# Kernel optimization log

Measured on AMD Instinct MI355X. Metric: run time of the kernel, lower is better.

Reference implementation:

```python
import jax, jax.numpy as jnp
import numpy as np

B, S, D, H = 2, 2048, 1024, 16
HD = D // H  # head_dim = 64


def setup_inputs() -> dict:
    key = jax.random.key(0)
    ks = jax.random.split(key, 6)
    scale = 1.0 / np.sqrt(D)
    x = jax.random.normal(ks[0], (B, S, D), dtype=jnp.float32)
    W_in = jax.random.normal(ks[1], (D, D), dtype=jnp.float32) * scale
    b_in = jnp.zeros((D,), dtype=jnp.float32)
    # per-head causal sequence-mixing weight, (H, S, S)
    W_mix = jax.random.normal(ks[2], (H, S, S), dtype=jnp.float32) / np.sqrt(S)
    W_out = jax.random.normal(ks[3], (D, D), dtype=jnp.float32) * scale
    b_out = jnp.zeros((D,), dtype=jnp.float32)
    index = S - 1  # python int; parallel form computes all indices at once
    return {"x": x, "W_in": W_in, "b_in": b_in, "W_mix": W_mix,
            "W_out": W_out, "b_out": b_out, "index": index}


def reference(x, W_in, b_in, W_mix, W_out, b_out, index):
    # in-projection (token-wise dense)
    xp = x @ W_in.T + b_in                      # (B, S, D)
    xh = xp.reshape(B, S, H, HD)                # split heads
    # causal (lower-triangular) per-head mixing over sequence positions
    causal = jnp.tril(jnp.ones((S, S), dtype=x.dtype))
    Wm = W_mix * causal                         # (H, S, S)
    # out[b,t,h,:] = sum_{j<=t} Wm[h,t,j] * xh[b,j,h,:]
    mixed = jnp.einsum('htj,bjhd->bthd', Wm, xh)
    out = mixed.reshape(B, S, D) @ W_out.T + b_out
    return out
```

## Files before the change

### kernel.cpp

```cpp
#include <hip/hip_runtime.h>
#include <hip/hip_bf16.h>
#include <stdint.h>

#define B_ 2
#define S_ 2048
#define D_ 1024
#define H_ 16
#define HD_ 64

typedef __attribute__((ext_vector_type(8))) short short8v;
typedef __attribute__((ext_vector_type(4))) float f32x4;
typedef __attribute__((ext_vector_type(4))) int int4v;

__device__ __forceinline__ unsigned short f2bf(float f) {
  union { float f; unsigned int u; } c; c.f = f;
  unsigned int u = c.u;
  unsigned int r = u + 0x7FFFu + ((u >> 16) & 1u);
  return (unsigned short)(r >> 16);
}

__device__ __forceinline__ void gload16(const void* g, void* l) {
  __builtin_amdgcn_global_load_lds(
      (const __attribute__((address_space(1))) unsigned int*)g,
      (__attribute__((address_space(3))) unsigned int*)l, 16, 0, 0);
}

#define NX4_ (B_ * S_ * D_ / 4)
#define NW4_ (D_ * D_ / 4)
__global__ __launch_bounds__(256) void convert3(
    const float* __restrict__ x, const float* __restrict__ wi, const float* __restrict__ wo,
    unsigned short* __restrict__ xb, unsigned short* __restrict__ wib,
    unsigned short* __restrict__ wob) {
  int i = blockIdx.x * 256 + threadIdx.x;
  const float* src; unsigned short* dst; int j;
  if (i < NX4_)              { src = x;  dst = xb;  j = i; }
  else if (i < NX4_ + NW4_)  { src = wi; dst = wib; j = i - NX4_; }
  else                       { src = wo; dst = wob; j = i - NX4_ - NW4_; }
  float4 v = reinterpret_cast<const float4*>(src)[j];
  ushort4 o;
  o.x = f2bf(v.x); o.y = f2bf(v.y); o.z = f2bf(v.z); o.w = f2bf(v.w);
  reinterpret_cast<ushort4*>(dst)[j] = o;
}

template<bool OUT_BF16>
__global__ __launch_bounds__(256) void gemm_bt(
    const unsigned short* __restrict__ A,
    const unsigned short* __restrict__ Bm,
    const float* __restrict__ bias,
    void* __restrict__ Cout,
    int M, int N, int K)
{
  __shared__ unsigned short As[128 * 32];
  __shared__ unsigned short Bs[128 * 32];
  const int tid = threadIdx.x;
  const int bM = blockIdx.y * 128, bN = blockIdx.x * 128;
  const int lane = tid & 63;
  const int w = tid >> 6;
  const int wr = (w >> 1) * 64;
  const int wc = (w & 1) * 64;
  const int lr = lane & 15, lk = (lane >> 4) * 8;
  const int srA = w * 32 + (lane >> 2);
  const int scs = (lane & 3) * 8;

  f32x4 acc[4][4] = {};

  for (int k0 = 0; k0 < K; k0 += 32) {
    gload16(A + (size_t)(bM + srA) * K + k0 + scs,      &As[srA * 32 + scs]);
    gload16(A + (size_t)(bM + srA + 16) * K + k0 + scs, &As[(srA + 16) * 32 + scs]);
    gload16(Bm + (size_t)(bN + srA) * K + k0 + scs,      &Bs[srA * 32 + scs]);
    gload16(Bm + (size_t)(bN + srA + 16) * K + k0 + scs, &Bs[(srA + 16) * 32 + scs]);
    __syncthreads();
    short8v av[4], bv[4];
#pragma unroll
    for (int m = 0; m < 4; m++)
      av[m] = *reinterpret_cast<const short8v*>(&As[(wr + m * 16 + lr) * 32 + lk]);
#pragma unroll
    for (int n = 0; n < 4; n++)
      bv[n] = *reinterpret_cast<const short8v*>(&Bs[(wc + n * 16 + lr) * 32 + lk]);
#pragma unroll
    for (int m = 0; m < 4; m++)
#pragma unroll
      for (int n = 0; n < 4; n++)
        acc[m][n] = __builtin_amdgcn_mfma_f32_16x16x32_bf16(av[m], bv[n], acc[m][n], 0, 0, 0);
    __syncthreads();
  }

  const int r0 = wr + (lane >> 4) * 4;
  const int c0 = wc + lr;
#pragma unroll
  for (int m = 0; m < 4; m++) {
#pragma unroll
    for (int n = 0; n < 4; n++) {
      const int gc = bN + c0 + n * 16;
      const float bb = bias[gc];
#pragma unroll
      for (int j = 0; j < 4; j++) {
        const int gr = bM + r0 + m * 16 + j;
        float v = acc[m][n][j] + bb;
        if (OUT_BF16)
          reinterpret_cast<unsigned short*>(Cout)[(size_t)gr * N + gc] = f2bf(v);
        else
          reinterpret_cast<float*>(Cout)[(size_t)gr * N + gc] = v;
      }
    }
  }
}

__global__ __launch_bounds__(256) void transpose_heads(
    const unsigned short* __restrict__ xp,
    unsigned short* __restrict__ xhT)
{
  const int bh = blockIdx.y;
  const int t0 = blockIdx.x * 64;
  const int b = bh >> 4, h = bh & 15;
  __shared__ unsigned short tile[64][72];
  const int tid = threadIdx.x;
  const int c8 = (tid & 7) * 8;
  const int r = tid >> 3;
  const size_t inBase = ((size_t)(b * S_ + t0)) * D_ + h * HD_;
#pragma unroll
  for (int p = 0; p < 2; p++) {
    const int tt = r + p * 32;
    *reinterpret_cast<int4v*>(&tile[tt][c8]) =
        *reinterpret_cast<const int4v*>(&xp[inBase + (size_t)tt * D_ + c8]);
  }
  __syncthreads();
#pragma unroll
  for (int p = 0; p < 2; p++) {
    const int d = r + p * 32;
    short8v v;
#pragma unroll
    for (int i = 0; i < 8; i++) v[i] = (short)tile[c8 + i][d];
    *reinterpret_cast<short8v*>(&xhT[((size_t)(bh * HD_) + d) * S_ + t0 + c8]) = v;
  }
}

template<bool MASK>
__device__ __forceinline__ short8v mix_fragA(const float* Asf, int rl, int lk, int k0, int T0) {
  f32x4 f0 = *reinterpret_cast<const f32x4*>(&Asf[rl * 32 + lk]);
  f32x4 f1 = *reinterpret_cast<const f32x4*>(&Asf[rl * 32 + lk + 4]);
  const int t = T0 + rl;
  short8v a;
#pragma unroll
  for (int e = 0; e < 4; e++) {
    float v0 = f0[e], v1 = f1[e];
    if (MASK) {
      if (k0 + lk + e > t)     v0 = 0.0f;
      if (k0 + lk + 4 + e > t) v1 = 0.0f;
    }
    a[e]     = (short)f2bf(v0);
    a[4 + e] = (short)f2bf(v1);
  }
  return a;
}

template<bool MASK>
__device__ __forceinline__ void mix_step(
    const float* Asf, const unsigned short* Bs, f32x4 (&acc)[2][4],
    int wr, int wc, int lr, int lk, int k0, int T0) {
  short8v av[2], bv[4];
#pragma unroll
  for (int m = 0; m < 2; m++)
    av[m] = mix_fragA<MASK>(Asf, wr + m * 16 + lr, lk, k0, T0);
#pragma unroll
  for (int n = 0; n < 4; n++)
    bv[n] = *reinterpret_cast<const short8v*>(&Bs[(wc + n * 16 + lr) * 32 + lk]);
#pragma unroll
  for (int m = 0; m < 2; m++)
#pragma unroll
    for (int n = 0; n < 4; n++)
      acc[m][n] = __builtin_amdgcn_mfma_f32_16x16x32_bf16(av[m], bv[n], acc[m][n], 0, 0, 0);
}

__global__ __launch_bounds__(256) void gemm_mix(
    const float* __restrict__ Wmix,
    const unsigned short* __restrict__ xhT,
    unsigned short* __restrict__ mixed)
{
  __shared__ float Asf[64 * 32];
  __shared__ unsigned short Bs[128 * 32];
  const int tid = threadIdx.x;
  const int h = blockIdx.y;
  const int xi = blockIdx.x;
  const int tilei = (xi & 1) ? (31 - (xi >> 1)) : (xi >> 1);
  const int T0 = tilei * 64;
  const int lane = tid & 63;
  const int w = tid >> 6;
  const int wr = (w >> 1) * 32;
  const int wc = (w & 1) * 64;
  const int lr = lane & 15, lk = (lane >> 4) * 8;
  const int arA = w * 16 + (lane >> 3);
  const int acf = (lane & 7) * 4;
  const int brA = w * 32 + (lane >> 2);
  const int bcs = (lane & 3) * 8;
  const int br0 = ((brA >> 6) * H_ + h) * HD_ + (brA & 63);
  const int br1 = (((brA + 16) >> 6) * H_ + h) * HD_ + ((brA + 16) & 63);

  f32x4 acc[2][4] = {};
  const float* Wh = Wmix + (size_t)h * S_ * S_;

  const int kMax = T0 + 64;
  for (int k0 = 0; k0 < kMax; k0 += 32) {
    gload16(Wh + (size_t)(T0 + arA) * S_ + k0 + acf,     &Asf[arA * 32 + acf]);
    gload16(Wh + (size_t)(T0 + arA + 8) * S_ + k0 + acf, &Asf[(arA + 8) * 32 + acf]);
    gload16(xhT + (size_t)br0 * S_ + k0 + bcs, &Bs[brA * 32 + bcs]);
    gload16(xhT + (size_t)br1 * S_ + k0 + bcs, &Bs[(brA + 16) * 32 + bcs]);
    __syncthreads();
    if (k0 + 32 > T0)
      mix_step<true>(Asf, Bs, acc, wr, wc, lr, lk, k0, T0);
    else
      mix_step<false>(Asf, Bs, acc, wr, wc, lr, lk, k0, T0);
    __syncthreads();
  }

  const int r0 = wr + (lane >> 4) * 4;
  const int c0 = wc + lr;
#pragma unroll
  for (int m = 0; m < 2; m++)
#pragma unroll
    for (int n = 0; n < 4; n++) {
      const int cc = c0 + n * 16;
      const int bb = cc >> 6, dd = cc & 63;
#pragma unroll
      for (int j = 0; j < 4; j++) {
        const int tt = T0 + r0 + m * 16 + j;
        mixed[((size_t)(bb * S_ + tt)) * D_ + h * HD_ + dd] = f2bf(acc[m][n][j]);
      }
    }
}

extern "C" void kernel_launch(void* const* d_in, const int* in_sizes, int n_in,
                              void* d_out, int out_size, void* d_ws, size_t ws_size,
                              hipStream_t stream) {
  const float* x     = (const float*)d_in[0];
  const float* W_in  = (const float*)d_in[1];
  const float* b_in  = (const float*)d_in[2];
  const float* W_mix = (const float*)d_in[3];
  const float* W_out = (const float*)d_in[4];
  const float* b_out = (const float*)d_in[5];

  char* ws = (char*)d_ws;
  unsigned short* xb    = (unsigned short*)(ws);
  unsigned short* xp    = (unsigned short*)(ws + 8u * 1024u * 1024u);
  unsigned short* wib   = (unsigned short*)(ws + 16u * 1024u * 1024u);
  unsigned short* wob   = (unsigned short*)(ws + 18u * 1024u * 1024u);
  unsigned short* xhT   = xb;
  unsigned short* mixed = xp;

  convert3<<<dim3((NX4_ + 2 * NW4_) / 256), dim3(256), 0, stream>>>(
      x, W_in, W_out, xb, wib, wob);

  gemm_bt<true><<<dim3(D_ / 128, B_ * S_ / 128), dim3(256), 0, stream>>>(
      xb, wib, b_in, (void*)xp, B_ * S_, D_, D_);

  transpose_heads<<<dim3(S_ / 64, B_ * H_), dim3(256), 0, stream>>>(xp, xhT);

  gemm_mix<<<dim3(S_ / 64, H_), dim3(256), 0, stream>>>(W_mix, xhT, mixed);

  gemm_bt<false><<<dim3(D_ / 128, B_ * S_ / 128), dim3(256), 0, stream>>>(
      mixed, wob, b_out, (void*)d_out, B_ * S_, D_, D_);
}
```

Baseline: 471.6 us.

## Drop LDS staging in GEMMs and fuse head transpose into in-projection

Replaces the LDS-staged GEMMs with register-only kernels that load MFMA fragments directly from global memory, using smaller 64x64 tiles. The in-projection now computes the transposed product W_in·x^T, so its output is already in the head-transposed layout and the separate transpose kernel is removed. The mixing kernel uses 32-row tiles with direct global loads and only masks the final diagonal step. The goal is to cut LDS traffic, barriers and one launch, at the cost of losing cross-wave operand reuse, which means many more redundant global and L2 reads, plus smaller per-wave tiles.

```diff
diff --git a/kernel.cpp b/kernel.cpp
--- a/kernel.cpp
+++ b/kernel.cpp
@@ -10,7 +10,6 @@
 
 typedef __attribute__((ext_vector_type(8))) short short8v;
 typedef __attribute__((ext_vector_type(4))) float f32x4;
-typedef __attribute__((ext_vector_type(4))) int int4v;
 
 __device__ __forceinline__ unsigned short f2bf(float f) {
   union { float f; unsigned int u; } c; c.f = f;
@@ -19,10 +18,8 @@
   return (unsigned short)(r >> 16);
 }
 
-__device__ __forceinline__ void gload16(const void* g, void* l) {
-  __builtin_amdgcn_global_load_lds(
-      (const __attribute__((address_space(1))) unsigned int*)g,
-      (__attribute__((address_space(3))) unsigned int*)l, 16, 0, 0);
+__device__ __forceinline__ f32x4 mfma16(short8v a, short8v b, f32x4 c) {
+  return __builtin_amdgcn_mfma_f32_16x16x32_bf16(a, b, c, 0, 0, 0);
 }
 
 #define NX4_ (B_ * S_ * D_ / 4)
@@ -42,61 +39,50 @@
   reinterpret_cast<ushort4*>(dst)[j] = o;
 }
 
-template<bool OUT_BF16>
-__global__ __launch_bounds__(256) void gemm_bt(
+template<bool OUT_BF16, bool BIAS_ROW>
+__global__ __launch_bounds__(256) void gemm_nolds(
     const unsigned short* __restrict__ A,
     const unsigned short* __restrict__ Bm,
     const float* __restrict__ bias,
-    void* __restrict__ Cout,
-    int M, int N, int K)
+    void* __restrict__ Cout, int M, int N, int K)
 {
-  __shared__ unsigned short As[128 * 32];
-  __shared__ unsigned short Bs[128 * 32];
   const int tid = threadIdx.x;
-  const int bM = blockIdx.y * 128, bN = blockIdx.x * 128;
   const int lane = tid & 63;
   const int w = tid >> 6;
-  const int wr = (w >> 1) * 64;
-  const int wc = (w & 1) * 64;
+  const int bM = blockIdx.y * 64, bN = blockIdx.x * 64;
+  const int wr = (w >> 1) * 32, wc = (w & 1) * 32;
   const int lr = lane & 15, lk = (lane >> 4) * 8;
-  const int srA = w * 32 + (lane >> 2);
-  const int scs = (lane & 3) * 8;
-
-  f32x4 acc[4][4] = {};
-
+
+  const unsigned short* a0 = A + (size_t)(bM + wr + lr) * K + lk;
+  const unsigned short* a1 = a0 + (size_t)16 * K;
+  const unsigned short* b0 = Bm + (size_t)(bN + wc + lr) * K + lk;
+  const unsigned short* b1 = b0 + (size_t)16 * K;
+
+  f32x4 acc[2][2] = {};
+#pragma unroll 2
   for (int k0 = 0; k0 < K; k0 += 32) {
-    gload16(A + (size_t)(bM + srA) * K + k0 + scs,      &As[srA * 32 + scs]);
-    gload16(A + (size_t)(bM + srA + 16) * K + k0 + scs, &As[(srA + 16) * 32 + scs]);
-    gload16(Bm + (size_t)(bN + srA) * K + k0 + scs,      &Bs[srA * 32 + scs]);
-    gload16(Bm + (size_t)(bN + srA + 16) * K + k0 + scs, &Bs[(srA + 16) * 32 + scs]);
-    __syncthreads();
-    short8v av[4], bv[4];
-#pragma unroll
-    for (int m = 0; m < 4; m++)
-      av[m] = *reinterpret_cast<const short8v*>(&As[(wr + m * 16 + lr) * 32 + lk]);
-#pragma unroll
-    for (int n = 0; n < 4; n++)
-      bv[n] = *reinterpret_cast<const short8v*>(&Bs[(wc + n * 16 + lr) * 32 + lk]);
-#pragma unroll
-    for (int m = 0; m < 4; m++)
-#pragma unroll
-      for (int n = 0; n < 4; n++)
-        acc[m][n] = __builtin_amdgcn_mfma_f32_16x16x32_bf16(av[m], bv[n], acc[m][n], 0, 0, 0);
-    __syncthreads();
+    short8v av0 = *reinterpret_cast<const short8v*>(a0 + k0);
+    short8v av1 = *reinterpret_cast<const short8v*>(a1 + k0);
+    short8v bv0 = *reinterpret_cast<const short8v*>(b0 + k0);
+    short8v bv1 = *reinterpret_cast<const short8v*>(b1 + k0);
+    acc[0][0] = mfma16(av0, bv0, acc[0][0]);
+    acc[0][1] = mfma16(av0, bv1, acc[0][1]);
+    acc[1][0] = mfma16(av1, bv0, acc[1][0]);
+    acc[1][1] = mfma16(av1, bv1, acc[1][1]);
   }
 
   const int r0 = wr + (lane >> 4) * 4;
   const int c0 = wc + lr;
 #pragma unroll
-  for (int m = 0; m < 4; m++) {
-#pragma unroll
-    for (int n = 0; n < 4; n++) {
+  for (int m = 0; m < 2; m++) {
+#pragma unroll
+    for (int n = 0; n < 2; n++) {
       const int gc = bN + c0 + n * 16;
-      const float bb = bias[gc];
+      float bcol = BIAS_ROW ? 0.0f : bias[gc];
 #pragma unroll
       for (int j = 0; j < 4; j++) {
         const int gr = bM + r0 + m * 16 + j;
-        float v = acc[m][n][j] + bb;
+        float v = acc[m][n][j] + (BIAS_ROW ? bias[gr] : bcol);
         if (OUT_BF16)
           reinterpret_cast<unsigned short*>(Cout)[(size_t)gr * N + gc] = f2bf(v);
         else
@@ -106,120 +92,90 @@
   }
 }
 
-__global__ __launch_bounds__(256) void transpose_heads(
-    const unsigned short* __restrict__ xp,
-    unsigned short* __restrict__ xhT)
-{
-  const int bh = blockIdx.y;
-  const int t0 = blockIdx.x * 64;
-  const int b = bh >> 4, h = bh & 15;
-  __shared__ unsigned short tile[64][72];
-  const int tid = threadIdx.x;
-  const int c8 = (tid & 7) * 8;
-  const int r = tid >> 3;
-  const size_t inBase = ((size_t)(b * S_ + t0)) * D_ + h * HD_;
-#pragma unroll
-  for (int p = 0; p < 2; p++) {
-    const int tt = r + p * 32;
-    *reinterpret_cast<int4v*>(&tile[tt][c8]) =
-        *reinterpret_cast<const int4v*>(&xp[inBase + (size_t)tt * D_ + c8]);
-  }
-  __syncthreads();
-#pragma unroll
-  for (int p = 0; p < 2; p++) {
-    const int d = r + p * 32;
-    short8v v;
-#pragma unroll
-    for (int i = 0; i < 8; i++) v[i] = (short)tile[c8 + i][d];
-    *reinterpret_cast<short8v*>(&xhT[((size_t)(bh * HD_) + d) * S_ + t0 + c8]) = v;
-  }
-}
-
-template<bool MASK>
-__device__ __forceinline__ short8v mix_fragA(const float* Asf, int rl, int lk, int k0, int T0) {
-  f32x4 f0 = *reinterpret_cast<const f32x4*>(&Asf[rl * 32 + lk]);
-  f32x4 f1 = *reinterpret_cast<const f32x4*>(&Asf[rl * 32 + lk + 4]);
-  const int t = T0 + rl;
-  short8v a;
+__device__ __forceinline__ short8v pack8(f32x4 lo, f32x4 hi) {
+  short8v r;
 #pragma unroll
   for (int e = 0; e < 4; e++) {
-    float v0 = f0[e], v1 = f1[e];
-    if (MASK) {
-      if (k0 + lk + e > t)     v0 = 0.0f;
-      if (k0 + lk + 4 + e > t) v1 = 0.0f;
-    }
-    a[e]     = (short)f2bf(v0);
-    a[4 + e] = (short)f2bf(v1);
-  }
-  return a;
-}
-
-template<bool MASK>
-__device__ __forceinline__ void mix_step(
-    const float* Asf, const unsigned short* Bs, f32x4 (&acc)[2][4],
-    int wr, int wc, int lr, int lk, int k0, int T0) {
-  short8v av[2], bv[4];
-#pragma unroll
-  for (int m = 0; m < 2; m++)
-    av[m] = mix_fragA<MASK>(Asf, wr + m * 16 + lr, lk, k0, T0);
-#pragma unroll
-  for (int n = 0; n < 4; n++)
-    bv[n] = *reinterpret_cast<const short8v*>(&Bs[(wc + n * 16 + lr) * 32 + lk]);
-#pragma unroll
-  for (int m = 0; m < 2; m++)
-#pragma unroll
-    for (int n = 0; n < 4; n++)
-      acc[m][n] = __builtin_amdgcn_mfma_f32_16x16x32_bf16(av[m], bv[n], acc[m][n], 0, 0, 0);
+    r[e]     = (short)f2bf(lo[e]);
+    r[4 + e] = (short)f2bf(hi[e]);
+  }
+  return r;
+}
+
+__device__ __forceinline__ short8v pack8_mask(f32x4 lo, f32x4 hi, int lk, int lim) {
+  short8v r;
+#pragma unroll
+  for (int e = 0; e < 4; e++) {
+    float v0 = (lk + e     <= lim) ? lo[e] : 0.0f;
+    float v1 = (lk + 4 + e <= lim) ? hi[e] : 0.0f;
+    r[e]     = (short)f2bf(v0);
+    r[4 + e] = (short)f2bf(v1);
+  }
+  return r;
 }
 
 __global__ __launch_bounds__(256) void gemm_mix(
     const float* __restrict__ Wmix,
-    const unsigned short* __restrict__ xhT,
+    const unsigned short* __restrict__ xpT,
     unsigned short* __restrict__ mixed)
 {
-  __shared__ float Asf[64 * 32];
-  __shared__ unsigned short Bs[128 * 32];
   const int tid = threadIdx.x;
+  const int lane = tid & 63;
+  const int w = tid >> 6;
   const int h = blockIdx.y;
   const int xi = blockIdx.x;
-  const int tilei = (xi & 1) ? (31 - (xi >> 1)) : (xi >> 1);
-  const int T0 = tilei * 64;
-  const int lane = tid & 63;
-  const int w = tid >> 6;
-  const int wr = (w >> 1) * 32;
-  const int wc = (w & 1) * 64;
+  const int tilei = (xi & 1) ? (63 - (xi >> 1)) : (xi >> 1);
+  const int T0 = tilei * 32;
+  const int wc = w * 32;
   const int lr = lane & 15, lk = (lane >> 4) * 8;
-  const int arA = w * 16 + (lane >> 3);
-  const int acf = (lane & 7) * 4;
-  const int brA = w * 32 + (lane >> 2);
-  const int bcs = (lane & 3) * 8;
-  const int br0 = ((brA >> 6) * H_ + h) * HD_ + (brA & 63);
-  const int br1 = (((brA + 16) >> 6) * H_ + h) * HD_ + ((brA + 16) & 63);
-
-  f32x4 acc[2][4] = {};
-  const float* Wh = Wmix + (size_t)h * S_ * S_;
-
-  const int kMax = T0 + 64;
-  for (int k0 = 0; k0 < kMax; k0 += 32) {
-    gload16(Wh + (size_t)(T0 + arA) * S_ + k0 + acf,     &Asf[arA * 32 + acf]);
-    gload16(Wh + (size_t)(T0 + arA + 8) * S_ + k0 + acf, &Asf[(arA + 8) * 32 + acf]);
-    gload16(xhT + (size_t)br0 * S_ + k0 + bcs, &Bs[brA * 32 + bcs]);
-    gload16(xhT + (size_t)br1 * S_ + k0 + bcs, &Bs[(brA + 16) * 32 + bcs]);
-    __syncthreads();
-    if (k0 + 32 > T0)
-      mix_step<true>(Asf, Bs, acc, wr, wc, lr, lk, k0, T0);
-    else
-      mix_step<false>(Asf, Bs, acc, wr, wc, lr, lk, k0, T0);
-    __syncthreads();
-  }
-
-  const int r0 = wr + (lane >> 4) * 4;
-  const int c0 = wc + lr;
+
+  const float* aw0 = Wmix + ((size_t)h * S_ + T0 + lr) * S_ + lk;
+  const float* aw1 = aw0 + (size_t)16 * S_;
+  const int cc0 = wc + lr, cc1 = wc + 16 + lr;
+  const unsigned short* bp0 =
+      xpT + ((size_t)(h * HD_) + (cc0 & 63)) * (B_ * S_) + (cc0 >> 6) * S_ + lk;
+  const unsigned short* bp1 =
+      xpT + ((size_t)(h * HD_) + (cc1 & 63)) * (B_ * S_) + (cc1 >> 6) * S_ + lk;
+
+  f32x4 acc[2][2] = {};
+
+#pragma unroll 2
+  for (int k0 = 0; k0 < T0; k0 += 32) {
+    f32x4 a00 = *reinterpret_cast<const f32x4*>(aw0 + k0);
+    f32x4 a01 = *reinterpret_cast<const f32x4*>(aw0 + k0 + 4);
+    f32x4 a10 = *reinterpret_cast<const f32x4*>(aw1 + k0);
+    f32x4 a11 = *reinterpret_cast<const f32x4*>(aw1 + k0 + 4);
+    short8v av0 = pack8(a00, a01);
+    short8v av1 = pack8(a10, a11);
+    short8v bv0 = *reinterpret_cast<const short8v*>(bp0 + k0);
+    short8v bv1 = *reinterpret_cast<const short8v*>(bp1 + k0);
+    acc[0][0] = mfma16(av0, bv0, acc[0][0]);
+    acc[0][1] = mfma16(av0, bv1, acc[0][1]);
+    acc[1][0] = mfma16(av1, bv0, acc[1][0]);
+    acc[1][1] = mfma16(av1, bv1, acc[1][1]);
+  }
+  {
+    const int k0 = T0;
+    f32x4 a00 = *reinterpret_cast<const f32x4*>(aw0 + k0);
+    f32x4 a01 = *reinterpret_cast<const f32x4*>(aw0 + k0 + 4);
+    f32x4 a10 = *reinterpret_cast<const f32x4*>(aw1 + k0);
+    f32x4 a11 = *reinterpret_cast<const f32x4*>(aw1 + k0 + 4);
+    short8v av0 = pack8_mask(a00, a01, lk, lr);
+    short8v av1 = pack8_mask(a10, a11, lk, 16 + lr);
+    short8v bv0 = *reinterpret_cast<const short8v*>(bp0 + k0);
+    short8v bv1 = *reinterpret_cast<const short8v*>(bp1 + k0);
+    acc[0][0] = mfma16(av0, bv0, acc[0][0]);
+    acc[0][1] = mfma16(av0, bv1, acc[0][1]);
+    acc[1][0] = mfma16(av1, bv0, acc[1][0]);
+    acc[1][1] = mfma16(av1, bv1, acc[1][1]);
+  }
+
+  const int r0 = (lane >> 4) * 4;
 #pragma unroll
   for (int m = 0; m < 2; m++)
 #pragma unroll
-    for (int n = 0; n < 4; n++) {
-      const int cc = c0 + n * 16;
+    for (int n = 0; n < 2; n++) {
+      const int cc = wc + lr + n * 16;
       const int bb = cc >> 6, dd = cc & 63;
 #pragma unroll
       for (int j = 0; j < 4; j++) {
@@ -241,22 +197,19 @@
 
   char* ws = (char*)d_ws;
   unsigned short* xb    = (unsigned short*)(ws);
-  unsigned short* xp    = (unsigned short*)(ws + 8u * 1024u * 1024u);
+  unsigned short* xpT   = (unsigned short*)(ws + 8u * 1024u * 1024u);
   unsigned short* wib   = (unsigned short*)(ws + 16u * 1024u * 1024u);
   unsigned short* wob   = (unsigned short*)(ws + 18u * 1024u * 1024u);
-  unsigned short* xhT   = xb;
-  unsigned short* mixed = xp;
+  unsigned short* mixed = xb;
 
   convert3<<<dim3((NX4_ + 2 * NW4_) / 256), dim3(256), 0, stream>>>(
       x, W_in, W_out, xb, wib, wob);
 
-  gemm_bt<true><<<dim3(D_ / 128, B_ * S_ / 128), dim3(256), 0, stream>>>(
-      xb, wib, b_in, (void*)xp, B_ * S_, D_, D_);
-
-  transpose_heads<<<dim3(S_ / 64, B_ * H_), dim3(256), 0, stream>>>(xp, xhT);
-
-  gemm_mix<<<dim3(S_ / 64, H_), dim3(256), 0, stream>>>(W_mix, xhT, mixed);
-
-  gemm_bt<false><<<dim3(D_ / 128, B_ * S_ / 128), dim3(256), 0, stream>>>(
+  gemm_nolds<true, true><<<dim3(B_ * S_ / 64, D_ / 64), dim3(256), 0, stream>>>(
+      wib, xb, b_in, (void*)xpT, D_, B_ * S_, D_);
+
+  gemm_mix<<<dim3(S_ / 32, H_), dim3(256), 0, stream>>>(W_mix, xpT, mixed);
+
+  gemm_nolds<false, false><<<dim3(D_ / 64, B_ * S_ / 64), dim3(256), 0, stream>>>(
       mixed, wob, b_out, (void*)d_out, B_ * S_, D_, D_);
 }
```

Measured after the change: 603.4 us. 27.9% more time.
